# Performance work log

Measured on AMD Instinct MI355X. Metric: run time of the kernel, lower is better.

Reference implementation:

```python
import jax, jax.numpy as jnp
import numpy as np

D_MODEL = 1024
N_HEADS = 16
ALPHA = 0.7
C_PARAM = 5
CUTOFF = C_PARAM // 2 + 1  # 3
LN_EPS = 1e-12
B, S = 4, 2048


def setup_inputs() -> dict:
    key = jax.random.key(0)
    ks = jax.random.split(key, 10)
    d = D_MODEL
    scale = 1.0 / np.sqrt(d)
    return {
        "input_tensor": jax.random.normal(ks[0], (B, S, d), dtype=jnp.float32),
        "attention_mask": jnp.ones((1, 1, S, S), dtype=jnp.int32),
        "sqrt_beta": jax.random.normal(ks[1], (1, 1, d), dtype=jnp.float32),
        "ln_gamma": jnp.ones((d,), dtype=jnp.float32),
        "ln_beta": jnp.zeros((d,), dtype=jnp.float32),
        "q_w": jax.random.normal(ks[2], (d, d), dtype=jnp.float32) * scale,
        "q_b": jnp.zeros((d,), dtype=jnp.float32),
        "k_w": jax.random.normal(ks[3], (d, d), dtype=jnp.float32) * scale,
        "k_b": jnp.zeros((d,), dtype=jnp.float32),
        "v_w": jax.random.normal(ks[4], (d, d), dtype=jnp.float32) * scale,
        "v_b": jnp.zeros((d,), dtype=jnp.float32),
    }


def _layer_norm(x, g, b):
    mu = jnp.mean(x, axis=-1, keepdims=True)
    var = jnp.mean(jnp.square(x - mu), axis=-1, keepdims=True)
    return (x - mu) * jax.lax.rsqrt(var + LN_EPS) * g + b


def bsarec_layer(x, mask, sqrt_beta, ln_gamma, ln_beta, q_w, q_b, k_w, k_b, v_w, v_b):
    batch, seq_len, hidden = x.shape
    # ---- FrequencyLayer (DSP branch) ----
    xf = jnp.fft.rfft(x, axis=1, norm='ortho')                 # [B, S//2+1, D]
    freq = jnp.arange(xf.shape[1])[None, :, None]
    low_pass = jnp.fft.irfft(jnp.where(freq < CUTOFF, xf, 0.0), n=seq_len, axis=1, norm='ortho')
    high_pass = x - low_pass
    seq_fft = low_pass + jnp.square(sqrt_beta) * high_pass
    dsp = _layer_norm(seq_fft + x, ln_gamma, ln_beta)          # dropout=0 -> identity
    # ---- MultiHeadAttention (GSP branch) ----
    h, d_k = N_HEADS, hidden // N_HEADS
    def split(t):  # [B,S,D] -> [B,H,S,d_k]
        return t.reshape(batch, seq_len, h, d_k).transpose(0, 2, 1, 3)
    q = split(x @ q_w.T + q_b)
    k = split(x @ k_w.T + k_b)
    v = split(x @ v_w.T + v_b)
    scores = jnp.einsum('bhsd,bhtd->bhst', q, k) / jnp.sqrt(jnp.float32(d_k))
    scores = jnp.where(mask == 0, -jnp.inf, scores)
    scores = scores - jnp.max(scores)                           # global max, as in source
    p = jax.nn.softmax(scores, axis=-1)
    p = jnp.where(jnp.isnan(p), 0.0, p)
    out = jnp.einsum('bhst,bhtd->bhsd', p, v)
    gsp = out.transpose(0, 2, 1, 3).reshape(batch, seq_len, hidden)
    return ALPHA * dsp + (1.0 - ALPHA) * gsp


def reference(input_tensor, attention_mask, sqrt_beta, ln_gamma, ln_beta, q_w, q_b, k_w, k_b, v_w, v_b):
    return bsarec_layer(input_tensor, attention_mask, sqrt_beta, ln_gamma, ln_beta,
                        q_w, q_b, k_w, k_b, v_w, v_b)
```

## Files before the change

### kernel.cpp

```cpp
#include <hip/hip_runtime.h>

#define S_LEN 2048
#define DM 1024
#define NB 4
#define NROWS (NB * S_LEN)
#define NHEADS 16
#define DK 64

typedef __bf16 bf16x8 __attribute__((ext_vector_type(8)));
typedef __bf16 bf16x2 __attribute__((ext_vector_type(2)));
typedef float f32x4 __attribute__((ext_vector_type(4)));
typedef float f32x2 __attribute__((ext_vector_type(2)));
typedef unsigned u32x4 __attribute__((ext_vector_type(4)));

struct __align__(8) us4 { unsigned short x, y, z, w; };

__device__ __forceinline__ unsigned cvt2(float a, float b) {
    f32x2 t; t.x = a; t.y = b;
    bf16x2 h = __builtin_convertvector(t, bf16x2);
    return __builtin_bit_cast(unsigned, h);
}
__device__ __forceinline__ unsigned short f2bf(float f) {
    __bf16 h = (__bf16)f;
    return __builtin_bit_cast(unsigned short, h);
}

__device__ __forceinline__ void gl2lds16(const void* g, void* l) {
    __builtin_amdgcn_global_load_lds(
        (const __attribute__((address_space(1))) unsigned int*)g,
        (__attribute__((address_space(3))) unsigned int*)l, 16, 0, 0);
}

#if __has_builtin(__builtin_amdgcn_exp2f)
#define EXP2F(x) __builtin_amdgcn_exp2f(x)
#else
#define EXP2F(x) exp2f(x)
#endif

__global__ __launch_bounds__(256) void prep(
    const float* __restrict__ x, float* __restrict__ coef,
    unsigned short* __restrict__ xbf, const float* __restrict__ qw,
    const float* __restrict__ kw, const float* __restrict__ vw,
    unsigned short* __restrict__ wbf) {
    int bx = blockIdx.x;
    if (bx >= 512) {
        int idx = ((bx - 512) * 256 + threadIdx.x) * 2;
        int which = idx >> 20, off = idx & 0xFFFFF;
        const float* src = (which == 0) ? qw : ((which == 1) ? kw : vw);
        float2 v = *(const float2*)(&src[off]);
        *(unsigned*)(&wbf[idx]) = cvt2(v.x, v.y);
        return;
    }
    int b = bx >> 7, dc = (bx >> 5) & 3, tc = bx & 31;
    int d = dc * 256 + threadIdx.x;
    __shared__ float tw[4][64];
    if (threadIdx.x < 64) {
        const float omega = 6.283185307179586476925f / (float)S_LEN;
        float sn, cs;
        __sincosf(omega * (float)(tc * 64 + threadIdx.x), &sn, &cs);
        tw[0][threadIdx.x] = sn;
        tw[1][threadIdx.x] = cs;
        tw[2][threadIdx.x] = 2.f * sn * cs;
        tw[3][threadIdx.x] = cs * cs - sn * sn;
    }
    __syncthreads();
    float c0 = 0.f, c1 = 0.f, s1 = 0.f, c2 = 0.f, s2 = 0.f;
    for (int i = 0; i < 64; ++i) {
        int t = tc * 64 + i;
        long idx = (long)(b * S_LEN + t) * DM + d;
        float v = x[idx];
        xbf[idx] = f2bf(v);
        c0 += v;
        c1 += v * tw[1][i];
        s1 += v * tw[0][i];
        c2 += v * tw[3][i];
        s2 += v * tw[2][i];
    }
    int base = b * DM + d;
    atomicAdd(&coef[0 * 4096 + base], c0);
    atomicAdd(&coef[1 * 4096 + base], c1);
    atomicAdd(&coef[2 * 4096 + base], s1);
    atomicAdd(&coef[3 * 4096 + base], c2);
    atomicAdd(&coef[4 * 4096 + base], s2);
}

__global__ __launch_bounds__(256) void dsp_ln(
    const float* __restrict__ x, const float* __restrict__ coef,
    const float* __restrict__ sqrt_beta, const float* __restrict__ gamma,
    const float* __restrict__ beta, const unsigned short* __restrict__ Og,
    float* __restrict__ out) {
    int row = blockIdx.x;
    int b = row >> 11, t = row & (S_LEN - 1);
    int tid = threadIdx.x, lane = tid & 63, wave = tid >> 6;
    const float omega = 6.283185307179586476925f / (float)S_LEN;
    float sn, cs;
    __sincosf(omega * (float)t, &sn, &cs);
    float c2t = cs * cs - sn * sn, s2t = 2.f * sn * cs;
    int d0 = tid * 4;
    long base = (long)row * DM;
    float4 xv = *(const float4*)(&x[base + d0]);
    int cb = b * DM + d0;
    float4 C0 = *(const float4*)(&coef[0 * 4096 + cb]);
    float4 C1 = *(const float4*)(&coef[1 * 4096 + cb]);
    float4 S1 = *(const float4*)(&coef[2 * 4096 + cb]);
    float4 C2 = *(const float4*)(&coef[3 * 4096 + cb]);
    float4 S2 = *(const float4*)(&coef[4 * 4096 + cb]);
    float4 sb = *(const float4*)(&sqrt_beta[d0]);
    const float inv_s = 1.0f / (float)S_LEN;
    float y[4];
#pragma unroll
    for (int i = 0; i < 4; ++i) {
        float c0 = (&C0.x)[i], c1 = (&C1.x)[i], s1 = (&S1.x)[i],
              c2 = (&C2.x)[i], s2 = (&S2.x)[i];
        float lp = (c0 + 2.f * (c1 * cs + s1 * sn) + 2.f * (c2 * c2t + s2 * s2t)) * inv_s;
        float xx = (&xv.x)[i];
        float b2 = (&sb.x)[i];
        b2 = b2 * b2;
        y[i] = xx + lp + b2 * (xx - lp);
    }
    float ssum = y[0] + y[1] + y[2] + y[3];
    float ssq = y[0] * y[0] + y[1] * y[1] + y[2] * y[2] + y[3] * y[3];
#pragma unroll
    for (int m = 1; m < 64; m <<= 1) {
        ssum += __shfl_xor(ssum, m, 64);
        ssq += __shfl_xor(ssq, m, 64);
    }
    __shared__ float red[8];
    if (lane == 0) { red[wave] = ssum; red[4 + wave] = ssq; }
    __syncthreads();
    float S = red[0] + red[1] + red[2] + red[3];
    float SQ = red[4] + red[5] + red[6] + red[7];
    float mu = S * (1.0f / DM);
    float var = SQ * (1.0f / DM) - mu * mu;
    float rstd = rsqrtf(var + 1e-12f);
    float4 g = *(const float4*)(&gamma[d0]);
    float4 be = *(const float4*)(&beta[d0]);
    us4 gv = *(const us4*)(&Og[((long)((b << 4) + (d0 >> 6)) * S_LEN + t) * DK + (d0 & 63)]);
    const unsigned short* gp = (const unsigned short*)&gv;
    float4 o;
#pragma unroll
    for (int i = 0; i < 4; ++i)
        (&o.x)[i] = 0.7f * ((y[i] - mu) * rstd * (&g.x)[i] + (&be.x)[i]) +
                    0.3f * __uint_as_float((unsigned)gp[i] << 16);
    *(float4*)(&out[base + d0]) = o;
}

__global__ __launch_bounds__(256) void gemm_qkv(
    const unsigned short* __restrict__ A, const unsigned short* __restrict__ W,
    const float* __restrict__ qb, const float* __restrict__ kb,
    const float* __restrict__ vb, unsigned short* __restrict__ Qo,
    unsigned short* __restrict__ Ko, unsigned short* __restrict__ Vt_g) {
    const int m0 = blockIdx.y * 128;
    const int n0g = blockIdx.x * 128;
    const int which = n0g >> 10;
    const int n0 = n0g & 1023;
    const int tid = threadIdx.x;
    const int lane = tid & 63, wave = tid >> 6;
    const int wm = wave >> 1, wn = wave & 1;
    const int r = lane & 15, q = lane >> 4;
    __shared__ __align__(16) unsigned short Sm[8192];
    unsigned short* As = Sm;
    unsigned short* Bs = Sm + 4096;
    const int lrow = lane >> 2;
    const int lch = (lane & 3) * 8;
    f32x4 acc[4][4] = {};
    for (int k0 = 0; k0 < DM; k0 += 32) {
        __syncthreads();
#pragma unroll
        for (int e = 0; e < 2; ++e) {
            int blk = e * 4 + wave;
            int row = blk * 16 + lrow;
            gl2lds16(&A[(long)(m0 + row) * DM + k0 + lch], &As[blk * 512 + lane * 8]);
            gl2lds16(&W[(long)(n0g + row) * DM + k0 + lch], &Bs[blk * 512 + lane * 8]);
        }
        __syncthreads();
        bf16x8 af[4], bfr[4];
#pragma unroll
        for (int i = 0; i < 4; ++i) {
            af[i] = *(const bf16x8*)(&As[(wm * 64 + i * 16 + r) * 32 + q * 8]);
            bfr[i] = *(const bf16x8*)(&Bs[(wn * 64 + i * 16 + r) * 32 + q * 8]);
        }
#pragma unroll
        for (int mi = 0; mi < 4; ++mi)
#pragma unroll
            for (int ni = 0; ni < 4; ++ni)
                acc[mi][ni] = __builtin_amdgcn_mfma_f32_16x16x32_bf16(
                    af[mi], bfr[ni], acc[mi][ni], 0, 0, 0);
    }
    const float* bias = (which == 0) ? qb : ((which == 1) ? kb : vb);
    if (which < 2) {
        const float qs = (which == 0) ? 0.18033688011112042f : 1.0f;
        unsigned short* Out = (which == 0) ? Qo : Ko;
#pragma unroll
        for (int p = 0; p < 4; ++p) {
            __syncthreads();
            if (wm == (p >> 1)) {
#pragma unroll
                for (int mi2 = 0; mi2 < 2; ++mi2) {
                    int mi = (p & 1) * 2 + mi2;
                    int rowL = mi2 * 16 + q * 4;
#pragma unroll
                    for (int ni = 0; ni < 4; ++ni) {
                        int col = wn * 64 + ni * 16 + r;
                        float bv = bias[n0 + col];
#pragma unroll
                        for (int reg = 0; reg < 4; ++reg)
                            Sm[(rowL + reg) * 134 + col] = f2bf((acc[mi][ni][reg] + bv) * qs);
                    }
                }
            }
            __syncthreads();
            int rowL = wave * 8 + (lane >> 3);
            int cc = (lane & 7) * 16;
            uint4 w0 = *(const uint4*)(&Sm[rowL * 134 + cc]);
            uint4 w1 = *(const uint4*)(&Sm[rowL * 134 + cc + 8]);
            long gb = (long)(m0 + p * 32 + rowL) * DM + n0 + cc;
            *(uint4*)(&Out[gb]) = w0;
            *(uint4*)(&Out[gb + 8]) = w1;
        }
    } else {
        const int bb = m0 >> 11, sg = m0 & (S_LEN - 1);
#pragma unroll
        for (int p = 0; p < 4; ++p) {
            __syncthreads();
            if (wn == (p >> 1)) {
#pragma unroll
                for (int ni2 = 0; ni2 < 2; ++ni2) {
                    int ni = (p & 1) * 2 + ni2;
                    int colL = ni2 * 16 + r;
                    float bv = bias[n0 + p * 32 + colL];
#pragma unroll
                    for (int mi = 0; mi < 4; ++mi) {
                        int s = wm * 64 + mi * 16 + q * 4;
                        *(unsigned*)(&Sm[colL * 134 + s]) =
                            cvt2(acc[mi][ni][0] + bv, acc[mi][ni][1] + bv);
                        *(unsigned*)(&Sm[colL * 134 + s + 2]) =
                            cvt2(acc[mi][ni][2] + bv, acc[mi][ni][3] + bv);
                    }
                }
            }
            __syncthreads();
            int colL = wave * 8 + (lane >> 3);
            int sc = (lane & 7) * 16;
            uint4 w0 = *(const uint4*)(&Sm[colL * 134 + sc]);
            uint4 w1 = *(const uint4*)(&Sm[colL * 134 + sc + 8]);
            long gb = ((long)bb * DM + n0 + p * 32 + colL) * S_LEN + sg + sc;
            *(uint4*)(&Vt_g[gb]) = w0;
            *(uint4*)(&Vt_g[gb + 8]) = w1;
        }
    }
}

__global__ __launch_bounds__(256, 2) void attn(
    const unsigned short* __restrict__ Q, const unsigned short* __restrict__ K,
    const unsigned short* __restrict__ Vt_g, unsigned short* __restrict__ Og) {
    int bx = blockIdx.x;
    int bh = bx & 63, qt = bx >> 6;
    int b = bh >> 4, h = bh & 15;
    const int tid = threadIdx.x, lane = tid & 63, wave = tid >> 6;
    const int r = lane & 15, q = lane >> 4;
    const int hc = h * DK;
    const int q0 = qt * 256 + wave * 64;

    bf16x8 aq[4][2];
#pragma unroll
    for (int mt = 0; mt < 4; ++mt) {
        long rowQ = (long)(b * S_LEN + q0 + mt * 16 + r) * DM + hc;
        aq[mt][0] = *(const bf16x8*)(&Q[rowQ + q * 8]);
        aq[mt][1] = *(const bf16x8*)(&Q[rowQ + 32 + q * 8]);
    }

    __shared__ __align__(16) unsigned short Ks[2][4096];
    __shared__ __align__(16) unsigned short Vt[2][4096];
    __shared__ float denL[256];

    f32x4 accO[4][4] = {};
    float den[4] = {};

    const int lr = lane >> 3, lc = lane & 7;
    const int cw0 = wave * 2, cw1 = cw0 + 1;
    const int ld0 = cw0 * 512, ld1 = cw1 * 512;
    const int row0 = cw0 * 8 + lr, row1 = cw1 * 8 + lr;
    const int cg0 = lc ^ lr;
    const int cg1 = lc ^ lr ^ 4;
    const unsigned short* kp0 = K + (long)(b * S_LEN + row0) * DM + hc + cg0 * 8;
    const unsigned short* kp1 = K + (long)(b * S_LEN + row1) * DM + hc + cg1 * 8;
    const unsigned short* vp0 = Vt_g + (long)(bh * 64 + row0) * S_LEN + cg0 * 8;
    const unsigned short* vp1 = Vt_g + (long)(bh * 64 + row1) * S_LEN + cg1 * 8;

    const int lo = r & 3, hi = r >> 2;
    const int abase = (hi * 8 + lo) * 64;
    const int ca = (q ^ lo ^ ((hi & 1) << 2)) * 8;
    const int cb2 = ca ^ 32;
    const int va0 = (q ^ (r & 7) ^ (((r >> 3) & 1) << 2)) * 8;
    const int va1 = va0 ^ 32;

#define STAGE(buf)                                    \
    do {                                              \
        gl2lds16(kp0, &Ks[buf][ld0 + lane * 8]);      \
        gl2lds16(kp1, &Ks[buf][ld1 + lane * 8]);      \
        gl2lds16(vp0, &Vt[buf][ld0 + lane * 8]);      \
        gl2lds16(vp1, &Vt[buf][ld1 + lane * 8]);      \
        kp0 += 64 * DM; kp1 += 64 * DM; vp0 += 64; vp1 += 64; \
    } while (0)

    STAGE(0);
    asm volatile("s_waitcnt vmcnt(0)" ::: "memory");
    __builtin_amdgcn_s_barrier();

    for (int t = 0; t < 32; ++t) {
        const int cur = t & 1;
        if (t < 31) STAGE(cur ^ 1);
        const unsigned short* Kc = Ks[cur];
        const unsigned short* Vc = Vt[cur];
        __builtin_amdgcn_s_setprio(1);
#pragma unroll
        for (int c = 0; c < 2; ++c) {
            const int cb64 = c * 2048;
            bf16x8 ak00 = *(const bf16x8*)(&Kc[cb64 + abase + ca]);
            bf16x8 ak01 = *(const bf16x8*)(&Kc[cb64 + abase + cb2]);
            bf16x8 ak10 = *(const bf16x8*)(&Kc[cb64 + 256 + abase + cb2]);
            bf16x8 ak11 = *(const bf16x8*)(&Kc[cb64 + 256 + abase + ca]);
            const int va = c ? va1 : va0;
            bf16x8 bv[4];
            bv[0] = *(const bf16x8*)(&Vc[(0 * 16 + r) * 64 + va]);
            bv[1] = *(const bf16x8*)(&Vc[(1 * 16 + r) * 64 + va]);
            bv[2] = *(const bf16x8*)(&Vc[(2 * 16 + r) * 64 + va]);
            bv[3] = *(const bf16x8*)(&Vc[(3 * 16 + r) * 64 + va]);
#pragma unroll
            for (int mt = 0; mt < 4; ++mt) {
                f32x4 sa = {}, sb = {};
                sa = __builtin_amdgcn_mfma_f32_16x16x32_bf16(ak00, aq[mt][0], sa, 0, 0, 0);
                sa = __builtin_amdgcn_mfma_f32_16x16x32_bf16(ak01, aq[mt][1], sa, 0, 0, 0);
                sb = __builtin_amdgcn_mfma_f32_16x16x32_bf16(ak10, aq[mt][0], sb, 0, 0, 0);
                sb = __builtin_amdgcn_mfma_f32_16x16x32_bf16(ak11, aq[mt][1], sb, 0, 0, 0);
                float p0 = EXP2F(sa[0]), p1 = EXP2F(sa[1]);
                float p2 = EXP2F(sa[2]), p3 = EXP2F(sa[3]);
                float p4 = EXP2F(sb[0]), p5 = EXP2F(sb[1]);
                float p6 = EXP2F(sb[2]), p7 = EXP2F(sb[3]);
                den[mt] += ((p0 + p1) + (p2 + p3)) + ((p4 + p5) + (p6 + p7));
                u32x4 wv;
                wv.x = cvt2(p0, p1); wv.y = cvt2(p2, p3);
                wv.z = cvt2(p4, p5); wv.w = cvt2(p6, p7);
                bf16x8 ap = __builtin_bit_cast(bf16x8, wv);
#pragma unroll
                for (int dt = 0; dt < 4; ++dt)
                    accO[mt][dt] = __builtin_amdgcn_mfma_f32_16x16x32_bf16(
                        ap, bv[dt], accO[mt][dt], 0, 0, 0);
            }
        }
        __builtin_amdgcn_s_setprio(0);
        asm volatile("s_waitcnt vmcnt(0)" ::: "memory");
        __builtin_amdgcn_s_barrier();
    }
#undef STAGE

#pragma unroll
    for (int mt = 0; mt < 4; ++mt) {
        float d = den[mt];
        d += __shfl_xor(d, 16, 64);
        d += __shfl_xor(d, 32, 64);
        if (q == 0) denL[wave * 64 + mt * 16 + r] = d;
    }
#pragma unroll
    for (int mt = 0; mt < 4; ++mt) {
        float4 dv = *(const float4*)(&denL[wave * 64 + mt * 16 + q * 4]);
        float rs[4];
#pragma unroll
        for (int reg = 0; reg < 4; ++reg) rs[reg] = 1.0f / (&dv.x)[reg];
        long obase = (long)bh * S_LEN + q0 + mt * 16 + q * 4;
#pragma unroll
        for (int dt = 0; dt < 4; ++dt) {
            int col = dt * 16 + r;
#pragma unroll
            for (int reg = 0; reg < 4; ++reg)
                Og[(obase + reg) * DK + col] = f2bf(accO[mt][dt][reg] * rs[reg]);
        }
    }
}

extern "C" void kernel_launch(void* const* d_in, const int* in_sizes, int n_in,
                              void* d_out, int out_size, void* d_ws, size_t ws_size,
                              hipStream_t stream) {
    const float* x = (const float*)d_in[0];
    const float* sqrt_beta = (const float*)d_in[2];
    const float* gamma = (const float*)d_in[3];
    const float* beta = (const float*)d_in[4];
    const float* qw = (const float*)d_in[5];
    const float* qb = (const float*)d_in[6];
    const float* kw = (const float*)d_in[7];
    const float* kb = (const float*)d_in[8];
    const float* vw = (const float*)d_in[9];
    const float* vb = (const float*)d_in[10];
    float* out = (float*)d_out;

    char* ws = (char*)d_ws;
    float* coef = (float*)ws;
    unsigned short* xbf = (unsigned short*)(ws + 81920);
    unsigned short* wbf = (unsigned short*)(ws + 81920 + 16777216);
    unsigned short* Qb = (unsigned short*)(ws + 81920 + 16777216 + 6291456);
    unsigned short* Kb = Qb + (long)NROWS * DM;
    unsigned short* Vt_g = Kb + (long)NROWS * DM;
    unsigned short* Og = xbf;

    hipMemsetAsync(coef, 0, 5 * 4096 * sizeof(float), stream);
    prep<<<6656, 256, 0, stream>>>(x, coef, xbf, qw, kw, vw, wbf);
    dim3 ggrid(3 * DM / 128, NROWS / 128);
    gemm_qkv<<<ggrid, 256, 0, stream>>>(xbf, wbf, qb, kb, vb, Qb, Kb, Vt_g);
    attn<<<NB * NHEADS * (S_LEN / 256), 256, 0, stream>>>(Qb, Kb, Vt_g, Og);
    dsp_ln<<<NROWS, 256, 0, stream>>>(x, coef, sqrt_beta, gamma, beta, Og, out);
}
```

Baseline: 275.1 us.

## Double-buffer QKV GEMM LDS tiles with XOR swizzle and MFMA priority

Restructures the QKV projection GEMM main loop to double-buffer the shared-memory A/W tiles, issuing the next k-slice's global-to-LDS loads before the current slice's MFMAs so load latency overlaps compute, with one barrier per iteration instead of two. Adds an XOR swizzle of 16-byte chunks within each 32-element row to reduce LDS bank conflicts on the fragment reads, and raises wave priority around the MFMA block. Doubles LDS use per block, which can lower occupancy. The epilogue still reuses Sm and relies on its own barriers, so correctness depends on the final loop barrier.

```diff
diff --git a/kernel.cpp b/kernel.cpp
--- a/kernel.cpp
+++ b/kernel.cpp
@@ -158,35 +158,51 @@
     const int lane = tid & 63, wave = tid >> 6;
     const int wm = wave >> 1, wn = wave & 1;
     const int r = lane & 15, q = lane >> 4;
-    __shared__ __align__(16) unsigned short Sm[8192];
-    unsigned short* As = Sm;
-    unsigned short* Bs = Sm + 4096;
+    __shared__ __align__(16) unsigned short Sm[16384];
     const int lrow = lane >> 2;
-    const int lch = (lane & 3) * 8;
+    const int swc = ((lane & 3) ^ (lrow & 3)) * 8;
+    const int rsw = (q ^ (r & 3)) * 8;
     f32x4 acc[4][4] = {};
-    for (int k0 = 0; k0 < DM; k0 += 32) {
-        __syncthreads();
-#pragma unroll
-        for (int e = 0; e < 2; ++e) {
-            int blk = e * 4 + wave;
-            int row = blk * 16 + lrow;
-            gl2lds16(&A[(long)(m0 + row) * DM + k0 + lch], &As[blk * 512 + lane * 8]);
-            gl2lds16(&W[(long)(n0g + row) * DM + k0 + lch], &Bs[blk * 512 + lane * 8]);
+
+#define GSTAGE(buf, k0)                                                  \
+    do {                                                                 \
+        _Pragma("unroll")                                                \
+        for (int e = 0; e < 2; ++e) {                                    \
+            int blk = e * 4 + wave;                                      \
+            int row = blk * 16 + lrow;                                   \
+            gl2lds16(&A[(long)(m0 + row) * DM + (k0) + swc],             \
+                     &Sm[(buf) * 4096 + blk * 512 + lane * 8]);          \
+            gl2lds16(&W[(long)(n0g + row) * DM + (k0) + swc],            \
+                     &Sm[8192 + (buf) * 4096 + blk * 512 + lane * 8]);   \
+        }                                                                \
+    } while (0)
+
+    GSTAGE(0, 0);
+    asm volatile("s_waitcnt vmcnt(0)" ::: "memory");
+    __builtin_amdgcn_s_barrier();
+    for (int it = 0; it < 32; ++it) {
+        const int cur = it & 1;
+        if (it < 31) GSTAGE(cur ^ 1, (it + 1) * 32);
+        const unsigned short* Ac = &Sm[cur * 4096];
+        const unsigned short* Bc = &Sm[8192 + cur * 4096];
+        bf16x8 af[4], bfr[4];
+#pragma unroll
+        for (int i = 0; i < 4; ++i) {
+            af[i]  = *(const bf16x8*)(&Ac[(wm * 64 + i * 16 + r) * 32 + rsw]);
+            bfr[i] = *(const bf16x8*)(&Bc[(wn * 64 + i * 16 + r) * 32 + rsw]);
         }
-        __syncthreads();
-        bf16x8 af[4], bfr[4];
-#pragma unroll
-        for (int i = 0; i < 4; ++i) {
-            af[i] = *(const bf16x8*)(&As[(wm * 64 + i * 16 + r) * 32 + q * 8]);
-            bfr[i] = *(const bf16x8*)(&Bs[(wn * 64 + i * 16 + r) * 32 + q * 8]);
-        }
+        __builtin_amdgcn_s_setprio(1);
 #pragma unroll
         for (int mi = 0; mi < 4; ++mi)
 #pragma unroll
             for (int ni = 0; ni < 4; ++ni)
                 acc[mi][ni] = __builtin_amdgcn_mfma_f32_16x16x32_bf16(
                     af[mi], bfr[ni], acc[mi][ni], 0, 0, 0);
-    }
+        __builtin_amdgcn_s_setprio(0);
+        asm volatile("s_waitcnt vmcnt(0)" ::: "memory");
+        __builtin_amdgcn_s_barrier();
+    }
+#undef GSTAGE
     const float* bias = (which == 0) ? qb : ((which == 1) ? kb : vb);
     if (which < 2) {
         const float qs = (which == 0) ? 0.18033688011112042f : 1.0f;
```

Result: faster. 269.3 us (-2.1%).

## Rewrite QKV GEMM with 256x256 tiles, 4-stage LDS pipeline and swizzle

Applied to the files above, without the earlier changes.

The QKV projection GEMM moves from 128x128 tiles with 4 waves to 256x256 tiles with 8 waves, and uses a 4-slot LDS ring buffer that prefetches two k-steps ahead with explicit vmcnt waits and raw barriers. LDS rows are XOR-swizzled to cut bank conflicts, and s_setprio is raised around the MFMA block. The aim is to hide global-to-LDS latency and raise arithmetic intensity per block. In exchange it uses 128 KB of LDS per block and more accumulator registers, and the grid shrinks to 384 blocks, which may lower occupancy or leave CUs idle.

```diff
diff --git a/kernel.cpp b/kernel.cpp
--- a/kernel.cpp
+++ b/kernel.cpp
@@ -145,108 +145,141 @@
     *(float4*)(&out[base + d0]) = o;
 }
 
-__global__ __launch_bounds__(256) void gemm_qkv(
+__global__ __launch_bounds__(512, 2) void gemm_qkv(
     const unsigned short* __restrict__ A, const unsigned short* __restrict__ W,
     const float* __restrict__ qb, const float* __restrict__ kb,
     const float* __restrict__ vb, unsigned short* __restrict__ Qo,
     unsigned short* __restrict__ Ko, unsigned short* __restrict__ Vt_g) {
-    const int m0 = blockIdx.y * 128;
-    const int n0g = blockIdx.x * 128;
+    const int m0 = blockIdx.y * 256;
+    const int n0g = blockIdx.x * 256;
     const int which = n0g >> 10;
     const int n0 = n0g & 1023;
     const int tid = threadIdx.x;
     const int lane = tid & 63, wave = tid >> 6;
-    const int wm = wave >> 1, wn = wave & 1;
+    const int wm = wave >> 2, wn = wave & 3;
     const int r = lane & 15, q = lane >> 4;
-    __shared__ __align__(16) unsigned short Sm[8192];
-    unsigned short* As = Sm;
-    unsigned short* Bs = Sm + 4096;
-    const int lrow = lane >> 2;
-    const int lch = (lane & 3) * 8;
-    f32x4 acc[4][4] = {};
-    for (int k0 = 0; k0 < DM; k0 += 32) {
-        __syncthreads();
-#pragma unroll
-        for (int e = 0; e < 2; ++e) {
-            int blk = e * 4 + wave;
-            int row = blk * 16 + lrow;
-            gl2lds16(&A[(long)(m0 + row) * DM + k0 + lch], &As[blk * 512 + lane * 8]);
-            gl2lds16(&W[(long)(n0g + row) * DM + k0 + lch], &Bs[blk * 512 + lane * 8]);
-        }
-        __syncthreads();
-        bf16x8 af[4], bfr[4];
-#pragma unroll
-        for (int i = 0; i < 4; ++i) {
-            af[i] = *(const bf16x8*)(&As[(wm * 64 + i * 16 + r) * 32 + q * 8]);
-            bfr[i] = *(const bf16x8*)(&Bs[(wn * 64 + i * 16 + r) * 32 + q * 8]);
-        }
-#pragma unroll
-        for (int mi = 0; mi < 4; ++mi)
-#pragma unroll
-            for (int ni = 0; ni < 4; ++ni)
-                acc[mi][ni] = __builtin_amdgcn_mfma_f32_16x16x32_bf16(
-                    af[mi], bfr[ni], acc[mi][ni], 0, 0, 0);
-    }
+    __shared__ __align__(16) unsigned short SmF[4 * 16384];
+    const int scol = ((lane & 3) ^ ((lane >> 3) & 3)) * 8;
+    const int rs = (q ^ ((r >> 1) & 3)) * 8;
+    f32x4 acc[8][4] = {};
+
+#define GST(slot_, kt_)                                                     \
+    do {                                                                    \
+        const int ko_ = (kt_) * 32;                                         \
+        _Pragma("unroll")                                                   \
+        for (int e = 0; e < 2; ++e) {                                       \
+            int cA = e * 8 + wave;                                          \
+            int grow = cA * 16 + (lane >> 2);                               \
+            gl2lds16(&A[(long)(m0 + grow) * DM + ko_ + scol],               \
+                     &SmF[(slot_) * 16384 + cA * 512 + lane * 8]);          \
+            gl2lds16(&W[(long)(n0g + grow) * DM + ko_ + scol],              \
+                     &SmF[(slot_) * 16384 + 8192 + cA * 512 + lane * 8]);   \
+        }                                                                   \
+    } while (0)
+
+    GST(0, 0);
+    GST(1, 1);
+    asm volatile("s_waitcnt vmcnt(4)" ::: "memory");
+    __builtin_amdgcn_s_barrier();
+
+    for (int kti = 0; kti < 32; ++kti) {
+        const int slot = kti & 3;
+        if (kti < 30) GST((kti + 2) & 3, kti + 2);
+        const unsigned short* Ac = &SmF[slot * 16384];
+        const unsigned short* Bc = Ac + 8192;
+        bf16x8 bfr[4];
+#pragma unroll
+        for (int ni = 0; ni < 4; ++ni)
+            bfr[ni] = *(const bf16x8*)(&Bc[(wn * 64 + ni * 16 + r) * 32 + rs]);
+        __builtin_amdgcn_s_setprio(1);
+#pragma unroll
+        for (int mh = 0; mh < 2; ++mh) {
+            bf16x8 af[4];
+#pragma unroll
+            for (int i = 0; i < 4; ++i)
+                af[i] = *(const bf16x8*)(
+                    &Ac[(wm * 128 + (mh * 4 + i) * 16 + r) * 32 + rs]);
+#pragma unroll
+            for (int i = 0; i < 4; ++i)
+#pragma unroll
+                for (int ni = 0; ni < 4; ++ni)
+                    acc[mh * 4 + i][ni] = __builtin_amdgcn_mfma_f32_16x16x32_bf16(
+                        af[i], bfr[ni], acc[mh * 4 + i][ni], 0, 0, 0);
+        }
+        __builtin_amdgcn_s_setprio(0);
+        if (kti < 31) {
+            if (kti < 30) {
+                asm volatile("s_waitcnt vmcnt(4)" ::: "memory");
+            } else {
+                asm volatile("s_waitcnt vmcnt(0)" ::: "memory");
+            }
+            __builtin_amdgcn_s_barrier();
+        }
+    }
+#undef GST
+    __syncthreads();
+
     const float* bias = (which == 0) ? qb : ((which == 1) ? kb : vb);
     if (which < 2) {
         const float qs = (which == 0) ? 0.18033688011112042f : 1.0f;
         unsigned short* Out = (which == 0) ? Qo : Ko;
 #pragma unroll
-        for (int p = 0; p < 4; ++p) {
-            __syncthreads();
-            if (wm == (p >> 1)) {
-#pragma unroll
-                for (int mi2 = 0; mi2 < 2; ++mi2) {
-                    int mi = (p & 1) * 2 + mi2;
-                    int rowL = mi2 * 16 + q * 4;
+        for (int strip = 0; strip < 2; ++strip) {
+            if (strip) __syncthreads();
+            if (wm == strip) {
+#pragma unroll
+                for (int mi = 0; mi < 8; ++mi) {
+                    int row = mi * 16 + q * 4;
 #pragma unroll
                     for (int ni = 0; ni < 4; ++ni) {
                         int col = wn * 64 + ni * 16 + r;
                         float bv = bias[n0 + col];
 #pragma unroll
                         for (int reg = 0; reg < 4; ++reg)
-                            Sm[(rowL + reg) * 134 + col] = f2bf((acc[mi][ni][reg] + bv) * qs);
+                            SmF[(row + reg) * 264 + col] =
+                                f2bf((acc[mi][ni][reg] + bv) * qs);
                     }
                 }
             }
             __syncthreads();
-            int rowL = wave * 8 + (lane >> 3);
-            int cc = (lane & 7) * 16;
-            uint4 w0 = *(const uint4*)(&Sm[rowL * 134 + cc]);
-            uint4 w1 = *(const uint4*)(&Sm[rowL * 134 + cc + 8]);
-            long gb = (long)(m0 + p * 32 + rowL) * DM + n0 + cc;
-            *(uint4*)(&Out[gb]) = w0;
-            *(uint4*)(&Out[gb + 8]) = w1;
+#pragma unroll
+            for (int p = 0; p < 8; ++p) {
+                int row = p * 16 + wave * 2 + (lane >> 5);
+                int cc = (lane & 31) * 8;
+                uint4 v = *(const uint4*)(&SmF[row * 264 + cc]);
+                long gb = (long)(m0 + strip * 128 + row) * DM + n0 + cc;
+                *(uint4*)(&Out[gb]) = v;
+            }
         }
     } else {
         const int bb = m0 >> 11, sg = m0 & (S_LEN - 1);
 #pragma unroll
-        for (int p = 0; p < 4; ++p) {
-            __syncthreads();
-            if (wn == (p >> 1)) {
-#pragma unroll
-                for (int ni2 = 0; ni2 < 2; ++ni2) {
-                    int ni = (p & 1) * 2 + ni2;
-                    int colL = ni2 * 16 + r;
-                    float bv = bias[n0 + p * 32 + colL];
-#pragma unroll
-                    for (int mi = 0; mi < 4; ++mi) {
-                        int s = wm * 64 + mi * 16 + q * 4;
-                        *(unsigned*)(&Sm[colL * 134 + s]) =
+        for (int strip = 0; strip < 2; ++strip) {
+            if (strip) __syncthreads();
+            if (wm == strip) {
+#pragma unroll
+                for (int ni = 0; ni < 4; ++ni) {
+                    int col = wn * 64 + ni * 16 + r;
+                    float bv = bias[n0 + col];
+#pragma unroll
+                    for (int mi = 0; mi < 8; ++mi) {
+                        int row = mi * 16 + q * 4;
+                        *(unsigned*)(&SmF[col * 136 + row]) =
                             cvt2(acc[mi][ni][0] + bv, acc[mi][ni][1] + bv);
-                        *(unsigned*)(&Sm[colL * 134 + s + 2]) =
+                        *(unsigned*)(&SmF[col * 136 + row + 2]) =
                             cvt2(acc[mi][ni][2] + bv, acc[mi][ni][3] + bv);
                     }
                 }
             }
             __syncthreads();
-            int colL = wave * 8 + (lane >> 3);
-            int sc = (lane & 7) * 16;
-            uint4 w0 = *(const uint4*)(&Sm[colL * 134 + sc]);
-            uint4 w1 = *(const uint4*)(&Sm[colL * 134 + sc + 8]);
-            long gb = ((long)bb * DM + n0 + p * 32 + colL) * S_LEN + sg + sc;
-            *(uint4*)(&Vt_g[gb]) = w0;
-            *(uint4*)(&Vt_g[gb + 8]) = w1;
+#pragma unroll
+            for (int p = 0; p < 8; ++p) {
+                int n = p * 32 + wave * 4 + (lane >> 4);
+                int mcc = (lane & 15) * 8;
+                uint4 v = *(const uint4*)(&SmF[n * 136 + mcc]);
+                long gb = ((long)bb * DM + n0 + n) * S_LEN + sg + strip * 128 + mcc;
+                *(uint4*)(&Vt_g[gb]) = v;
+            }
         }
     }
 }
@@ -405,8 +438,8 @@
 
     hipMemsetAsync(coef, 0, 5 * 4096 * sizeof(float), stream);
     prep<<<6656, 256, 0, stream>>>(x, coef, xbf, qw, kw, vw, wbf);
-    dim3 ggrid(3 * DM / 128, NROWS / 128);
-    gemm_qkv<<<ggrid, 256, 0, stream>>>(xbf, wbf, qb, kb, vb, Qb, Kb, Vt_g);
+    dim3 ggrid(3 * DM / 256, NROWS / 256);
+    gemm_qkv<<<ggrid, 512, 0, stream>>>(xbf, wbf, qb, kb, vb, Qb, Kb, Vt_g);
     attn<<<NB * NHEADS * (S_LEN / 256), 256, 0, stream>>>(Qb, Kb, Vt_g, Og);
     dsp_ln<<<NROWS, 256, 0, stream>>>(x, coef, sqrt_beta, gamma, beta, Og, out);
 }
```

Measured after the change: 267.2 us. -2.9%, faster.
